# Kernel tuning notes

Measured on AMD Instinct MI355X. Metric: run time of the kernel, lower is better.

## Reference

```python
import jax, jax.numpy as jnp
import numpy as np


def setup_inputs() -> dict:
    key = jax.random.key(0)
    ks = jax.random.split(key, 4)
    B, T, M, E, F = 4, 2048, 1024, 8, 4096
    hidden_states = jax.random.normal(ks[0], (B, T, M), dtype=jnp.float32)
    wg = jax.random.normal(ks[1], (M, E), dtype=jnp.float32) * (1.0 / np.sqrt(M))
    w1 = jax.random.normal(ks[2], (E, M, F), dtype=jnp.float32) * (1.0 / np.sqrt(M))
    b1 = jnp.zeros((E, F), dtype=jnp.float32)
    w2 = jax.random.normal(ks[3], (E, F, M), dtype=jnp.float32) * (1.0 / np.sqrt(F))
    b2 = jnp.zeros((E, M), dtype=jnp.float32)
    return {"hidden_states": hidden_states, "wg": wg, "w1": w1, "b1": b1, "w2": w2, "b2": b2}


def reference(hidden_states, wg, w1, b1, w2, b2):
    B, T, M = hidden_states.shape
    E = wg.shape[1]
    S = B * T
    MIN_CAPACITY = 4
    C = max((S + E - 1) // E, MIN_CAPACITY)  # capacity_factor = 1 (static)

    x = hidden_states.reshape(S, M)  # [S, M]

    # --- top-1 gating (deepspeed TopKGate, noisy=None, use_rts=False) ---
    logits = x @ wg                                  # [S, E]
    gates = jax.nn.softmax(logits, axis=-1)          # [S, E]
    idx = jnp.argmax(gates, axis=-1)                 # [S]
    mask1 = jax.nn.one_hot(idx, E, dtype=gates.dtype)  # [S, E]
    # aux loss (computed before capacity drop)
    l_aux = jnp.sum(gates.mean(0) * mask1.mean(0)) * E
    # position of each token within its expert's queue
    locations1 = jnp.cumsum(mask1, axis=0) - 1.0     # [S, E]
    mask1 = mask1 * (locations1 < C)                 # drop overflow tokens
    gates1_s = jnp.sum(gates * mask1, axis=1)        # [S]
    loc_s = jnp.sum(locations1 * mask1, axis=1).astype(jnp.int32)  # [S]
    loc_sc = jax.nn.one_hot(loc_s, C, dtype=gates.dtype)           # [S, C]

    combine_weights = jnp.einsum('se,sc->sec', gates1_s[:, None] * mask1, loc_sc)  # [S,E,C]
    dispatch_mask = (combine_weights > 0).astype(x.dtype)

    # --- dispatch ---
    dispatched = jnp.einsum('sec,sm->ecm', dispatch_mask, x)  # [E, C, M]

    # --- expert FFN (grouped GEMM) ---
    h = jax.nn.gelu(jnp.einsum('ecm,emf->ecf', dispatched, w1) + b1[:, None, :])
    expert_out = jnp.einsum('ecf,efm->ecm', h, w2) + b2[:, None, :]  # [E, C, M]

    # --- combine ---
    out = jnp.einsum('sec,ecm->sm', combine_weights, expert_out)  # [S, M]
    return out.reshape(B, T, M)
```

## Files before the change

kernel.cpp:

```cpp
#include <hip/hip_runtime.h>
#include <hip/hip_bf16.h>
#include <math.h>

#define S_TOK 8192
#define M_DIM 1024
#define E_NUM 8
#define F_DIM 4096
#define CAP   1024

typedef short short8 __attribute__((ext_vector_type(8)));
typedef float f32x4 __attribute__((ext_vector_type(4)));
typedef unsigned short ushortx4 __attribute__((ext_vector_type(4)));

__device__ inline unsigned short f2bf(float f) {
    union { float f; unsigned int u; } v; v.f = f;
    unsigned int r = v.u + 0x7fffu + ((v.u >> 16) & 1u);
    return (unsigned short)(r >> 16);
}

__device__ inline float gelu_fast(float x) {
    float y = 0.7978845608028654f * (x + 0.044715f * x * x * x);
    if (y > 40.f) return x;
    float e = exp2f(2.8853900817779268f * y);
    return x * e / (e + 1.0f);
}

__device__ inline void gl_lds16(const void* g, void* l) {
    __builtin_amdgcn_global_load_lds(
        (const __attribute__((address_space(1))) unsigned int*)g,
        (__attribute__((address_space(3))) unsigned int*)l, 16, 0, 0);
}

__global__ __launch_bounds__(256) void gating_kernel(
    const float* __restrict__ x, const float* __restrict__ wg,
    int* __restrict__ idx, float* __restrict__ gate)
{
    int wid = threadIdx.x >> 6;
    int lane = threadIdx.x & 63;
    int s = blockIdx.x * 4 + wid;
    const float* xs = x + (size_t)s * M_DIM;

    double acc[E_NUM];
#pragma unroll
    for (int e = 0; e < E_NUM; e++) acc[e] = 0.0;

    for (int i = lane; i < M_DIM; i += 64) {
        float xv = xs[i];
        float4 wa = *(const float4*)(wg + (size_t)i * E_NUM);
        float4 wb = *(const float4*)(wg + (size_t)i * E_NUM + 4);
        acc[0] += (double)xv * (double)wa.x;
        acc[1] += (double)xv * (double)wa.y;
        acc[2] += (double)xv * (double)wa.z;
        acc[3] += (double)xv * (double)wa.w;
        acc[4] += (double)xv * (double)wb.x;
        acc[5] += (double)xv * (double)wb.y;
        acc[6] += (double)xv * (double)wb.z;
        acc[7] += (double)xv * (double)wb.w;
    }
#pragma unroll
    for (int e = 0; e < E_NUM; e++) {
        double v = acc[e];
        for (int o = 32; o > 0; o >>= 1) v += __shfl_down(v, o, 64);
        acc[e] = v;
    }
    if (lane == 0) {
        double mx = acc[0]; int am = 0;
#pragma unroll
        for (int e = 1; e < E_NUM; e++) {
            if (acc[e] > mx) { mx = acc[e]; am = e; }
        }
        double se = 0.0;
#pragma unroll
        for (int e = 0; e < E_NUM; e++) se += exp(acc[e] - mx);
        idx[s] = am;
        gate[s] = (float)(1.0 / se);
    }
}

__global__ __launch_bounds__(1024) void scan_build(
    const int* __restrict__ idx, int* __restrict__ srcmap)
{
    __shared__ unsigned int sc[2][4][1024];
    int t = threadIdx.x;

    for (int i = t; i < E_NUM * CAP; i += 1024) srcmap[i] = -1;

    int eid[8];
    unsigned int cnt[E_NUM];
#pragma unroll
    for (int e = 0; e < E_NUM; e++) cnt[e] = 0;
#pragma unroll
    for (int i = 0; i < 8; i++) {
        int e = idx[t * 8 + i];
        eid[i] = e;
        cnt[e]++;
    }
    unsigned int pk[4];
#pragma unroll
    for (int i = 0; i < 4; i++) pk[i] = cnt[2 * i] | (cnt[2 * i + 1] << 16);
#pragma unroll
    for (int i = 0; i < 4; i++) sc[0][i][t] = pk[i];

    int buf = 0;
    for (int ofs = 1; ofs < 1024; ofs <<= 1) {
        __syncthreads();
        unsigned int v[4];
#pragma unroll
        for (int i = 0; i < 4; i++) {
            v[i] = sc[buf][i][t] + ((t >= ofs) ? sc[buf][i][t - ofs] : 0u);
            sc[buf ^ 1][i][t] = v[i];
        }
        buf ^= 1;
    }
    __syncthreads();
    unsigned int pos[E_NUM];
#pragma unroll
    for (int e = 0; e < E_NUM; e++) {
        unsigned int incl = (sc[buf][e >> 1][t] >> ((e & 1) * 16)) & 0xffffu;
        pos[e] = incl - cnt[e];
    }
#pragma unroll
    for (int i = 0; i < 8; i++) {
        int e = eid[i];
        unsigned int p = pos[e]++;
        if (p < CAP) srcmap[e * CAP + p] = t * 8 + i;
    }
}

__global__ __launch_bounds__(256) void dispatch_kernel(
    const float* __restrict__ x, const int* __restrict__ srcmap,
    unsigned short* __restrict__ A1)
{
    int slot = blockIdx.x;
    int s = srcmap[slot];
    int t = threadIdx.x;
    ushortx4 o;
    if (s >= 0) {
        float4 v = ((const float4*)(x + (size_t)s * M_DIM))[t];
        o[0] = f2bf(v.x); o[1] = f2bf(v.y); o[2] = f2bf(v.z); o[3] = f2bf(v.w);
    } else {
        o[0] = 0; o[1] = 0; o[2] = 0; o[3] = 0;
    }
    ((ushortx4*)(A1 + (size_t)slot * M_DIM))[t] = o;
}

__global__ __launch_bounds__(256) void transpose_cvt(
    const float* __restrict__ in, unsigned short* __restrict__ out, int R, int Cc)
{
    __shared__ float tile[32][33];
    int e = blockIdx.z;
    int br = blockIdx.y * 32, bc = blockIdx.x * 32;
    const float* ine = in + (size_t)e * R * Cc;
    unsigned short* oute = out + (size_t)e * R * Cc;
    int tx = threadIdx.x, ty = threadIdx.y;
#pragma unroll
    for (int i = 0; i < 32; i += 8)
        tile[ty + i][tx] = ine[(size_t)(br + ty + i) * Cc + (bc + tx)];
    __syncthreads();
#pragma unroll
    for (int i = 0; i < 32; i += 8)
        oute[(size_t)(bc + ty + i) * R + (br + tx)] = f2bf(tile[tx][ty + i]);
}

template <int MODE>
__global__ __launch_bounds__(256, 3) void gemm128(
    const unsigned short* __restrict__ A, const unsigned short* __restrict__ B,
    const float* __restrict__ bias, unsigned short* __restrict__ OutH,
    float* __restrict__ OutF, const int* __restrict__ srcmap,
    const float* __restrict__ gate)
{
    constexpr int K   = (MODE == 0) ? 1024 : 4096;
    constexpr int NB  = (MODE == 0) ? 4096 : 1024;
    constexpr int NT  = K / 32;
    constexpr int NWG = (MODE == 0) ? 2048 : 512;

    __shared__ __align__(16) unsigned short LDS[3 * 8192];

    int bid = blockIdx.x;
    int swz = (bid & 7) * (NWG / 8) + (bid >> 3);
    int e, tm, tn;
    if (MODE == 0) { e = swz >> 8; int r = swz & 255; tn = r >> 3; tm = r & 7; }
    else           { e = swz >> 6; int r = swz & 63;  tn = r >> 3; tm = r & 7; }

    const unsigned short* Ae = A + ((size_t)e * CAP + (size_t)tm * 128) * K;
    const unsigned short* Be = B + ((size_t)e * NB + (size_t)tn * 128) * K;

    int tid = threadIdx.x, w = tid >> 6, lane = tid & 63;
    int wm = w >> 1, wn = w & 1;
    int fr = lane & 15, kq = lane >> 4;
    int r0 = wm * 64, c0 = wn * 64;

    int lr2 = lane >> 2, sl4 = lane & 3;
    int lc = sl4 ^ (lr2 & 3);
    const unsigned short* gA[2]; const unsigned short* gB[2]; int dA[2], dB[2];
#pragma unroll
    for (int i = 0; i < 2; i++) {
        int rb = w * 32 + i * 16;
        gA[i] = Ae + (size_t)(rb + lr2) * K + lc * 8;
        gB[i] = Be + (size_t)(rb + lr2) * K + lc * 8;
        dA[i] = rb * 32;
        dB[i] = 4096 + rb * 32;
    }

#define STAGE(sl, t_) do { int ko_ = (t_) * 32;                      \
    gl_lds16(gA[0] + ko_, &LDS[(sl) * 8192 + dA[0]]);                \
    gl_lds16(gA[1] + ko_, &LDS[(sl) * 8192 + dA[1]]);                \
    gl_lds16(gB[0] + ko_, &LDS[(sl) * 8192 + dB[0]]);                \
    gl_lds16(gB[1] + ko_, &LDS[(sl) * 8192 + dB[1]]);                \
} while (0)

    int swc = ((kq ^ (fr & 3)) << 3);
    int aoff = (r0 + fr) * 32 + swc;
    int boff = 4096 + (c0 + fr) * 32 + swc;

    f32x4 acc[4][4];
#pragma unroll
    for (int i = 0; i < 4; i++)
#pragma unroll
        for (int j = 0; j < 4; j++) acc[i][j] = (f32x4){0.f, 0.f, 0.f, 0.f};

    STAGE(0, 0);
    STAGE(1, 1);
    asm volatile("s_waitcnt vmcnt(4)" ::: "memory");
    __builtin_amdgcn_s_barrier();

    int cur = 0, stg = 2;
#pragma unroll 1
    for (int t = 0; t < NT; ++t) {
        if (t + 2 < NT) STAGE(stg, t + 2);

        int sb = cur * 8192;
        short8 a[4], b[4];
#pragma unroll
        for (int mi = 0; mi < 4; mi++)
            a[mi] = *(const short8*)&LDS[sb + aoff + mi * 512];
#pragma unroll
        for (int ni = 0; ni < 4; ni++)
            b[ni] = *(const short8*)&LDS[sb + boff + ni * 512];
        __builtin_amdgcn_s_setprio(1);
#pragma unroll
        for (int mi = 0; mi < 4; mi++)
#pragma unroll
            for (int ni = 0; ni < 4; ni++)
                acc[mi][ni] = __builtin_amdgcn_mfma_f32_16x16x32_bf16(
                    a[mi], b[ni], acc[mi][ni], 0, 0, 0);
        __builtin_amdgcn_s_setprio(0);

        if (t + 2 < NT)      asm volatile("s_waitcnt vmcnt(4)" ::: "memory");
        else if (t + 1 < NT) asm volatile("s_waitcnt vmcnt(0)" ::: "memory");
        __builtin_amdgcn_s_barrier();
        cur = (cur + 1 == 3) ? 0 : cur + 1;
        stg = (stg + 1 == 3) ? 0 : stg + 1;
    }
#undef STAGE

    if (MODE == 0) {
        unsigned short* R = (unsigned short*)LDS;
        float bv[4];
#pragma unroll
        for (int ni = 0; ni < 4; ni++)
            bv[ni] = bias[e * NB + tn * 128 + c0 + ni * 16 + fr];
#pragma unroll
        for (int mi = 0; mi < 4; mi++) {
#pragma unroll
            for (int j = 0; j < 4; j++) {
                int row = r0 + mi * 16 + kq * 4 + j;
#pragma unroll
                for (int ni = 0; ni < 4; ni++) {
                    int col = c0 + ni * 16 + fr;
                    R[row * 128 + (((col >> 3) ^ (row & 7)) << 3) + (col & 7)] =
                        f2bf(gelu_fast(acc[mi][ni][j] + bv[ni]));
                }
            }
        }
        __syncthreads();
        int row = tid >> 1, seg = tid & 1;
        size_t gb = ((size_t)(e * CAP + tm * 128 + row)) * NB + tn * 128 + seg * 64;
#pragma unroll
        for (int i = 0; i < 8; i++) {
            int chunk = seg * 8 + i;
            *(short8*)&OutH[gb + i * 8] =
                *(const short8*)&R[row * 128 + ((chunk ^ (row & 7)) << 3)];
        }
    } else {
        float bv[4];
#pragma unroll
        for (int ni = 0; ni < 4; ni++)
            bv[ni] = bias[e * NB + tn * 128 + c0 + ni * 16 + fr];
#pragma unroll
        for (int mi = 0; mi < 4; mi++) {
#pragma unroll
            for (int j = 0; j < 4; j++) {
                int r = tm * 128 + r0 + mi * 16 + kq * 4 + j;
                int s = srcmap[e * CAP + r];
                if (s < 0) continue;
                float g = gate[s];
                float* ob = OutF + (size_t)s * NB + tn * 128 + c0;
#pragma unroll
                for (int ni = 0; ni < 4; ni++)
                    ob[ni * 16 + fr] = g * (acc[mi][ni][j] + bv[ni]);
            }
        }
    }
}

extern "C" void kernel_launch(void* const* d_in, const int* in_sizes, int n_in,
                              void* d_out, int out_size, void* d_ws, size_t ws_size,
                              hipStream_t stream) {
    const float* x  = (const float*)d_in[0];
    const float* wg = (const float*)d_in[1];
    const float* w1 = (const float*)d_in[2];
    const float* b1 = (const float*)d_in[3];
    const float* w2 = (const float*)d_in[4];
    const float* b2 = (const float*)d_in[5];
    float* out = (float*)d_out;

    char* ws = (char*)d_ws;
    unsigned short* A1  = (unsigned short*)(ws);
    unsigned short* W1T = (unsigned short*)(ws + (size_t)(16u << 20));
    unsigned short* W2T = (unsigned short*)(ws + (size_t)(80u << 20));
    unsigned short* H   = (unsigned short*)(ws + (size_t)(144u << 20));
    int*   idx  = (int*)(ws + (size_t)(208u << 20));
    float* gate = (float*)(ws + (size_t)(208u << 20) + 32768);
    int*   srcm = (int*)(ws + (size_t)(208u << 20) + 65536);

    hipMemsetAsync(d_out, 0, (size_t)S_TOK * M_DIM * sizeof(float), stream);

    gating_kernel<<<S_TOK / 4, 256, 0, stream>>>(x, wg, idx, gate);
    scan_build<<<1, 1024, 0, stream>>>(idx, srcm);
    dispatch_kernel<<<E_NUM * CAP, 256, 0, stream>>>(x, srcm, A1);
    transpose_cvt<<<dim3(F_DIM / 32, M_DIM / 32, E_NUM), dim3(32, 8), 0, stream>>>(
        w1, W1T, M_DIM, F_DIM);
    transpose_cvt<<<dim3(M_DIM / 32, F_DIM / 32, E_NUM), dim3(32, 8), 0, stream>>>(
        w2, W2T, F_DIM, M_DIM);

    gemm128<0><<<2048, 256, 0, stream>>>(A1, W1T, b1, H, nullptr, nullptr, nullptr);

    gemm128<1><<<512, 256, 0, stream>>>(H, W2T, b2, nullptr, out, srcm, gate);
}
```

Before: 345.0 us.

## Use 256x128 GEMM tiles with split-K for the second expert GEMM

Both expert GEMMs now use 512-thread workgroups with 256x128 output tiles, which raises operand reuse per LDS stage (A is loaded twice per B stage). The down-projection GEMM is split into two K halves that write fp32 partial sums into the workspace, reusing the W1T region once it is no longer needed. A new combine kernel adds the two partials and the bias, applies the gate, and scatters each row to its token. This trades extra global traffic for the partial buffers, plus one more launch, for better MFMA density and more workgroups in flight on the second GEMM.

```diff
diff --git a/kernel.cpp b/kernel.cpp
--- a/kernel.cpp
+++ b/kernel.cpp
@@ -163,27 +163,33 @@
 }
 
 template <int MODE>
-__global__ __launch_bounds__(256, 3) void gemm128(
+__global__ __launch_bounds__(512, 4) void gemm256x128(
     const unsigned short* __restrict__ A, const unsigned short* __restrict__ B,
     const float* __restrict__ bias, unsigned short* __restrict__ OutH,
-    float* __restrict__ OutF, const int* __restrict__ srcmap,
-    const float* __restrict__ gate)
-{
-    constexpr int K   = (MODE == 0) ? 1024 : 4096;
-    constexpr int NB  = (MODE == 0) ? 4096 : 1024;
-    constexpr int NT  = K / 32;
-    constexpr int NWG = (MODE == 0) ? 2048 : 512;
-
-    __shared__ __align__(16) unsigned short LDS[3 * 8192];
+    float* __restrict__ OutP)
+{
+    constexpr int K    = (MODE == 0) ? 1024 : 4096;
+    constexpr int NB   = (MODE == 0) ? 4096 : 1024;
+    constexpr int KLEN = (MODE == 0) ? 1024 : 2048;
+    constexpr int NT   = KLEN / 32;
+    constexpr int NWG  = (MODE == 0) ? 1024 : 512;
+    constexpr int SLOT = 12288;
+
+    __shared__ __align__(16) unsigned short LDS[3 * SLOT];
 
     int bid = blockIdx.x;
     int swz = (bid & 7) * (NWG / 8) + (bid >> 3);
-    int e, tm, tn;
-    if (MODE == 0) { e = swz >> 8; int r = swz & 255; tn = r >> 3; tm = r & 7; }
-    else           { e = swz >> 6; int r = swz & 63;  tn = r >> 3; tm = r & 7; }
-
-    const unsigned short* Ae = A + ((size_t)e * CAP + (size_t)tm * 128) * K;
-    const unsigned short* Be = B + ((size_t)e * NB + (size_t)tn * 128) * K;
+    int e, tm, tn, ks;
+    if (MODE == 0) {
+        e = swz >> 7; int r = swz & 127; tn = r >> 2; tm = r & 3; ks = 0;
+    } else {
+        e = swz >> 6; int r = swz & 63; ks = r >> 5; int rr = r & 31;
+        tn = rr >> 2; tm = rr & 3;
+    }
+    int kOff = (MODE == 0) ? 0 : ks * 2048;
+
+    const unsigned short* Ae = A + ((size_t)e * CAP + (size_t)tm * 256) * K + kOff;
+    const unsigned short* Be = B + ((size_t)e * NB + (size_t)tn * 128) * K + kOff;
 
     int tid = threadIdx.x, w = tid >> 6, lane = tid & 63;
     int wm = w >> 1, wn = w & 1;
@@ -192,26 +198,22 @@
 
     int lr2 = lane >> 2, sl4 = lane & 3;
     int lc = sl4 ^ (lr2 & 3);
-    const unsigned short* gA[2]; const unsigned short* gB[2]; int dA[2], dB[2];
-#pragma unroll
-    for (int i = 0; i < 2; i++) {
-        int rb = w * 32 + i * 16;
-        gA[i] = Ae + (size_t)(rb + lr2) * K + lc * 8;
-        gB[i] = Be + (size_t)(rb + lr2) * K + lc * 8;
-        dA[i] = rb * 32;
-        dB[i] = 4096 + rb * 32;
-    }
+    const unsigned short* gA0 = Ae + (size_t)(w * 16 + lr2) * K + lc * 8;
+    const unsigned short* gA1 = Ae + (size_t)(128 + w * 16 + lr2) * K + lc * 8;
+    const unsigned short* gB  = Be + (size_t)(w * 16 + lr2) * K + lc * 8;
+    int dA0 = (w * 16) * 32;
+    int dA1 = (128 + w * 16) * 32;
+    int dB  = 8192 + (w * 16) * 32;
 
 #define STAGE(sl, t_) do { int ko_ = (t_) * 32;                      \
-    gl_lds16(gA[0] + ko_, &LDS[(sl) * 8192 + dA[0]]);                \
-    gl_lds16(gA[1] + ko_, &LDS[(sl) * 8192 + dA[1]]);                \
-    gl_lds16(gB[0] + ko_, &LDS[(sl) * 8192 + dB[0]]);                \
-    gl_lds16(gB[1] + ko_, &LDS[(sl) * 8192 + dB[1]]);                \
+    gl_lds16(gA0 + ko_, &LDS[(sl) * SLOT + dA0]);                    \
+    gl_lds16(gA1 + ko_, &LDS[(sl) * SLOT + dA1]);                    \
+    gl_lds16(gB  + ko_, &LDS[(sl) * SLOT + dB]);                     \
 } while (0)
 
     int swc = ((kq ^ (fr & 3)) << 3);
     int aoff = (r0 + fr) * 32 + swc;
-    int boff = 4096 + (c0 + fr) * 32 + swc;
+    int boff = 8192 + (c0 + fr) * 32 + swc;
 
     f32x4 acc[4][4];
 #pragma unroll
@@ -221,7 +223,7 @@
 
     STAGE(0, 0);
     STAGE(1, 1);
-    asm volatile("s_waitcnt vmcnt(4)" ::: "memory");
+    asm volatile("s_waitcnt vmcnt(3)" ::: "memory");
     __builtin_amdgcn_s_barrier();
 
     int cur = 0, stg = 2;
@@ -229,7 +231,7 @@
     for (int t = 0; t < NT; ++t) {
         if (t + 2 < NT) STAGE(stg, t + 2);
 
-        int sb = cur * 8192;
+        int sb = cur * SLOT;
         short8 a[4], b[4];
 #pragma unroll
         for (int mi = 0; mi < 4; mi++)
@@ -246,7 +248,7 @@
                     a[mi], b[ni], acc[mi][ni], 0, 0, 0);
         __builtin_amdgcn_s_setprio(0);
 
-        if (t + 2 < NT)      asm volatile("s_waitcnt vmcnt(4)" ::: "memory");
+        if (t + 2 < NT)      asm volatile("s_waitcnt vmcnt(3)" ::: "memory");
         else if (t + 1 < NT) asm volatile("s_waitcnt vmcnt(0)" ::: "memory");
         __builtin_amdgcn_s_barrier();
         cur = (cur + 1 == 3) ? 0 : cur + 1;
@@ -264,7 +266,7 @@
         for (int mi = 0; mi < 4; mi++) {
 #pragma unroll
             for (int j = 0; j < 4; j++) {
-                int row = r0 + mi * 16 + kq * 4 + j;
+                int row = wm * 64 + mi * 16 + kq * 4 + j;
 #pragma unroll
                 for (int ni = 0; ni < 4; ni++) {
                     int col = c0 + ni * 16 + fr;
@@ -275,7 +277,7 @@
         }
         __syncthreads();
         int row = tid >> 1, seg = tid & 1;
-        size_t gb = ((size_t)(e * CAP + tm * 128 + row)) * NB + tn * 128 + seg * 64;
+        size_t gb = ((size_t)(e * CAP + tm * 256 + row)) * NB + tn * 128 + seg * 64;
 #pragma unroll
         for (int i = 0; i < 8; i++) {
             int chunk = seg * 8 + i;
@@ -283,25 +285,41 @@
                 *(const short8*)&R[row * 128 + ((chunk ^ (row & 7)) << 3)];
         }
     } else {
-        float bv[4];
-#pragma unroll
-        for (int ni = 0; ni < 4; ni++)
-            bv[ni] = bias[e * NB + tn * 128 + c0 + ni * 16 + fr];
+        float* OP = OutP + (size_t)ks * S_TOK * M_DIM;
 #pragma unroll
         for (int mi = 0; mi < 4; mi++) {
 #pragma unroll
             for (int j = 0; j < 4; j++) {
-                int r = tm * 128 + r0 + mi * 16 + kq * 4 + j;
-                int s = srcmap[e * CAP + r];
-                if (s < 0) continue;
-                float g = gate[s];
-                float* ob = OutF + (size_t)s * NB + tn * 128 + c0;
+                int r = tm * 256 + wm * 64 + mi * 16 + kq * 4 + j;
+                size_t rowbase = ((size_t)(e * CAP + r)) * NB + tn * 128 + c0;
 #pragma unroll
                 for (int ni = 0; ni < 4; ni++)
-                    ob[ni * 16 + fr] = g * (acc[mi][ni][j] + bv[ni]);
+                    OP[rowbase + ni * 16 + fr] = acc[mi][ni][j];
             }
         }
     }
+}
+
+__global__ __launch_bounds__(256) void combine_kernel(
+    const float* __restrict__ P, const int* __restrict__ srcmap,
+    const float* __restrict__ gate, const float* __restrict__ b2,
+    float* __restrict__ out)
+{
+    int r = blockIdx.x;
+    int s = srcmap[r];
+    if (s < 0) return;
+    int e = r >> 10;
+    float g = gate[s];
+    int t = threadIdx.x;
+    float4 p0 = ((const float4*)P)[r * 256 + t];
+    float4 p1 = ((const float4*)(P + (size_t)S_TOK * M_DIM))[r * 256 + t];
+    float4 bb = ((const float4*)b2)[e * 256 + t];
+    float4 o;
+    o.x = g * (p0.x + p1.x + bb.x);
+    o.y = g * (p0.y + p1.y + bb.y);
+    o.z = g * (p0.z + p1.z + bb.z);
+    o.w = g * (p0.w + p1.w + bb.w);
+    ((float4*)out)[s * 256 + t] = o;
 }
 
 extern "C" void kernel_launch(void* const* d_in, const int* in_sizes, int n_in,
@@ -318,6 +336,7 @@
     char* ws = (char*)d_ws;
     unsigned short* A1  = (unsigned short*)(ws);
     unsigned short* W1T = (unsigned short*)(ws + (size_t)(16u << 20));
+    float*          P   = (float*)(ws + (size_t)(16u << 20));
     unsigned short* W2T = (unsigned short*)(ws + (size_t)(80u << 20));
     unsigned short* H   = (unsigned short*)(ws + (size_t)(144u << 20));
     int*   idx  = (int*)(ws + (size_t)(208u << 20));
@@ -334,7 +353,9 @@
     transpose_cvt<<<dim3(M_DIM / 32, F_DIM / 32, E_NUM), dim3(32, 8), 0, stream>>>(
         w2, W2T, F_DIM, M_DIM);
 
-    gemm128<0><<<2048, 256, 0, stream>>>(A1, W1T, b1, H, nullptr, nullptr, nullptr);
-
-    gemm128<1><<<512, 256, 0, stream>>>(H, W2T, b2, nullptr, out, srcm, gate);
-}
+    gemm256x128<0><<<1024, 512, 0, stream>>>(A1, W1T, b1, H, nullptr);
+
+    gemm256x128<1><<<512, 512, 0, stream>>>(H, W2T, nullptr, nullptr, P);
+
+    combine_kernel<<<E_NUM * CAP, 256, 0, stream>>>(P, srcm, gate, b2, out);
+}
```

Result: faster. 336.4 us (-2.5%).
